# Performance work log

Hardware: AMD Instinct MI355X
Metric: run time of the kernel (lower is better)

The kernel has to match this reference:

```python
import jax, jax.numpy as jnp
import numpy as np

VOCAB, HIDDEN, BATCH, EMB, SEQ = 512, 512, 64, 256, 1024


def _lstm_cell(x, h, c, Wih, Whh, bih, bhh):
    # PyTorch LSTMCell gate order: i, f, g, o
    gates = x @ Wih.T + bih + h @ Whh.T + bhh  # [B, 4H]
    i, f, g, o = jnp.split(gates, 4, axis=-1)
    i = jax.nn.sigmoid(i)
    f = jax.nn.sigmoid(f)
    g = jnp.tanh(g)
    o = jax.nn.sigmoid(o)
    c_new = f * c + i * g
    h_new = o * jnp.tanh(c_new)
    return h_new, c_new


def setup_inputs() -> dict:
    key = jax.random.key(0)
    ks = jax.random.split(key, 12)
    s_e = 1.0 / np.sqrt(HIDDEN)
    inp = {
        "x": jax.random.randint(ks[0], (SEQ, BATCH), 0, VOCAB, dtype=jnp.int64)
        if jax.config.jax_enable_x64 else jax.random.randint(ks[0], (SEQ, BATCH), 0, VOCAB, dtype=jnp.int32),
        "h0": jnp.zeros((BATCH, HIDDEN), jnp.float32),
        "c0": jnp.zeros((BATCH, HIDDEN), jnp.float32),
        "emb": jax.random.normal(ks[1], (VOCAB, EMB), jnp.float32),
        "Wih1": jax.random.uniform(ks[2], (4 * HIDDEN, EMB), jnp.float32, -s_e, s_e),
        "Whh1": jax.random.uniform(ks[3], (4 * HIDDEN, HIDDEN), jnp.float32, -s_e, s_e),
        "bih1": jax.random.uniform(ks[4], (4 * HIDDEN,), jnp.float32, -s_e, s_e),
        "bhh1": jax.random.uniform(ks[5], (4 * HIDDEN,), jnp.float32, -s_e, s_e),
        "Wih2": jax.random.uniform(ks[6], (4 * HIDDEN, HIDDEN), jnp.float32, -s_e, s_e),
        "Whh2": jax.random.uniform(ks[7], (4 * HIDDEN, HIDDEN), jnp.float32, -s_e, s_e),
        "bih2": jax.random.uniform(ks[8], (4 * HIDDEN,), jnp.float32, -s_e, s_e),
        "bhh2": jax.random.uniform(ks[9], (4 * HIDDEN,), jnp.float32, -s_e, s_e),
        "Wfc": jax.random.uniform(ks[10], (VOCAB, HIDDEN), jnp.float32, -s_e, s_e),
        "bfc": jax.random.uniform(ks[11], (VOCAB,), jnp.float32, -s_e, s_e),
    }
    return inp


def reference(x, h0, c0, emb, Wih1, Whh1, bih1, bhh1, Wih2, Whh2, bih2, bhh2, Wfc, bfc):
    # Embedding lookup for the whole sequence: [S, B, E]
    x_emb = emb[x]

    def step(carry, xt):
        h1, c1, h2, c2 = carry
        h1, c1 = _lstm_cell(xt, h1, c1, Wih1, Whh1, bih1, bhh1)
        h2, c2 = _lstm_cell(h1, h2, c2, Wih2, Whh2, bih2, bhh2)
        return (h1, c1, h2, c2), h2

    # Both layers start from the same (h0, c0), matching the original hc1, hc2 = (hc, hc)
    _, h2_seq = jax.lax.scan(step, (h0, c0, h0, c0), x_emb)  # [S, B, H]
    # Dropout is identity in eval mode; output projection over all timesteps at once.
    out = jnp.einsum('sbh,vh->sbv', h2_seq, Wfc) + bfc  # [S, B, V]
    return out
```

## Files before the change

kernel.cpp:

```cpp
#include <hip/hip_runtime.h>

#define SEQn   1024
#define BATCHn 64
#define EMBn   256
#define HIDn   512
#define VOCn   512

#define NGRP 4
#define NL1g 16
#define NL2g 16
#define NFCg 16
#define GBLK (NL1g + NL2g + NFCg)
#define NBLK (NGRP * GBLK)
#define NPHASE (SEQn + 2)
#define HS 8192

using f16   = _Float16;
using half8 = __attribute__((ext_vector_type(8))) _Float16;
using f32x4 = __attribute__((ext_vector_type(4))) float;
using i32x4 = __attribute__((ext_vector_type(4))) int;

#define WS_FLG 0
#define WS_H1  4096
#define WS_H2  (WS_H1 + NGRP * 4 * HS * 2)
#define WS_P1  (WS_H2 + NGRP * 4 * HS * 2)


__device__ __forceinline__ float sigm_(float v) { return 1.0f / (1.0f + __expf(-v)); }
__device__ __forceinline__ float tanh_(float v) { return 1.0f - 2.0f / (__expf(2.0f * v) + 1.0f); }

__device__ __forceinline__ void st_b128_sc1(f16* p, f32x4 v) {
  asm volatile("global_store_dwordx4 %0, %1, off sc1" :: "v"(p), "v"(v) : "memory");
}

__device__ __forceinline__ void ld2_sc1(const f16* base, half8 (&a)[2]) {
  f32x4 t0, t1;
  asm volatile(
    "global_load_dwordx4 %0, %2, off sc1\n\t"
    "global_load_dwordx4 %1, %2, off offset:1024 sc1\n\t"
    "s_waitcnt vmcnt(0)"
    : "=&v"(t0), "=&v"(t1) : "v"(base) : "memory");
  a[0] = __builtin_bit_cast(half8, t0);
  a[1] = __builtin_bit_cast(half8, t1);
}
__device__ __forceinline__ void ld4_sc1(const f16* base, half8 (&a)[4]) {
  f32x4 t0, t1, t2, t3;
  asm volatile(
    "global_load_dwordx4 %0, %4, off sc1\n\t"
    "global_load_dwordx4 %1, %4, off offset:1024 sc1\n\t"
    "global_load_dwordx4 %2, %4, off offset:2048 sc1\n\t"
    "global_load_dwordx4 %3, %4, off offset:3072 sc1\n\t"
    "s_waitcnt vmcnt(0)"
    : "=&v"(t0), "=&v"(t1), "=&v"(t2), "=&v"(t3) : "v"(base) : "memory");
  a[0] = __builtin_bit_cast(half8, t0);
  a[1] = __builtin_bit_cast(half8, t1);
  a[2] = __builtin_bit_cast(half8, t2);
  a[3] = __builtin_bit_cast(half8, t3);
}

__global__ void k_init(const float* __restrict__ h0, char* __restrict__ ws) {
  int i = blockIdx.x * 256 + threadIdx.x;
  f16* h1b = (f16*)(ws + WS_H1);
  f16* h2b = (f16*)(ws + WS_H2);
  int slice = i >> 13;
  int off = i & (HS - 1);
  int g = slice >> 2;
  int ks = off >> 9, rem = off & 511;
  int qq = rem >> 7, cc = (rem >> 3) & 15, e = rem & 7;
  int row = g * 16 + cc, col = ks * 32 + qq * 8 + e;
  f16 v = (f16)h0[row * HIDn + col];
  h1b[i] = v;
  h2b[i] = v;
  if (i < 1024) ((int*)ws)[i] = 0;
}

__global__ void k_p1(const float* __restrict__ emb, const float* __restrict__ Wih1,
                     const float* __restrict__ bih1, const float* __restrict__ bhh1,
                     char* __restrict__ ws) {
  __shared__ float elds[32 * 256];
  int tid = threadIdx.x;
  int vb = blockIdx.x >> 5, gb = blockIdx.x & 31;
  for (int i = tid; i < 32 * 256; i += 256) elds[i] = emb[vb * 32 * 256 + i];
  __syncthreads();
  int gl = tid & 63, vs = tid >> 6;
  int g = gb * 64 + gl;
  float bias = bih1[g] + bhh1[g];
  float acc[8];
#pragma unroll
  for (int r = 0; r < 8; ++r) acc[r] = bias;
  const float* wrow = Wih1 + g * EMBn;
#pragma unroll 4
  for (int e = 0; e < EMBn; ++e) {
    float w = wrow[e];
#pragma unroll
    for (int r = 0; r < 8; ++r) acc[r] += elds[(vs * 8 + r) * 256 + e] * w;
  }
  f16* P1 = (f16*)(ws + WS_P1);
#pragma unroll
  for (int r = 0; r < 8; ++r) P1[(vb * 32 + vs * 8 + r) * 2048 + g] = (f16)acc[r];
}

__global__ void __launch_bounds__(512, 2)
k_lstm(const int* __restrict__ x, const float* __restrict__ c0,
       const float* __restrict__ Whh1,
       const float* __restrict__ Wih2, const float* __restrict__ Whh2,
       const float* __restrict__ bih2, const float* __restrict__ bhh2,
       const float* __restrict__ Wfc, const float* __restrict__ bfc,
       float* __restrict__ out, char* __restrict__ ws)
{
  __shared__ float part[8][16][132];
  __shared__ alignas(16) f16 hstage[16][32];

  const int bid = blockIdx.x, tid = threadIdx.x;
  const int lane = tid & 63, wv = tid >> 6;
  const int cc = lane & 15, qq = lane >> 4;
  const int group = bid / GBLK, role = bid % GBLK;
  const int rp = role & 1;

  f16* h1g = (f16*)(ws + WS_H1) + group * 4 * HS;
  f16* h2g = (f16*)(ws + WS_H2) + group * 4 * HS;
  const f16* P1 = (const f16*)(ws + WS_P1);
  int* flagp = (int*)ws + (group << 6) + role;

  half8 bfr[32];
  float cst = 0.f;
  float biasr[4] = {0.f, 0.f, 0.f, 0.f};
  float bfcr = 0.f;
  float pgf[4] = {0.f, 0.f, 0.f, 0.f};
  int j0 = 0;
  const int erow = tid >> 5, eu = tid & 31;

  if (role < NL1g) {
    j0 = role * 32;
#pragma unroll
    for (int nt = 0; nt < 8; ++nt) {
      const float* wr = Whh1 + ((nt >> 1) * 512 + j0 + (nt & 1) * 16 + cc) * HIDn;
#pragma unroll
      for (int kk = 0; kk < 2; ++kk) {
        const float* s = wr + (wv * 2 + kk) * 32 + qq * 8;
        half8 hv;
#pragma unroll
        for (int j = 0; j < 8; ++j) hv[j] = (f16)s[j];
        bfr[nt * 2 + kk] = hv;
      }
    }
    cst = c0[(group * 16 + erow) * HIDn + j0 + eu];
    {
      const f16* pr = P1 + (size_t)x[group * 16 + erow] * 2048 + j0 + eu;
#pragma unroll
      for (int g = 0; g < 4; ++g) pgf[g] = (float)pr[g * 512];
    }
  } else if (role < NL1g + NL2g) {
    j0 = (role - NL1g) * 32;
    const int kh = wv >> 2, kq = wv & 3;
    const float* W = kh ? Whh2 : Wih2;
#pragma unroll
    for (int nt = 0; nt < 8; ++nt) {
      const float* wr = W + ((nt >> 1) * 512 + j0 + (nt & 1) * 16 + cc) * HIDn;
#pragma unroll
      for (int kk = 0; kk < 4; ++kk) {
        const float* s = wr + (kq * 4 + kk) * 32 + qq * 8;
        half8 hv;
#pragma unroll
        for (int j = 0; j < 8; ++j) hv[j] = (f16)s[j];
        bfr[nt * 4 + kk] = hv;
      }
    }
#pragma unroll
    for (int g = 0; g < 4; ++g)
      biasr[g] = bih2[g * 512 + j0 + eu] + bhh2[g * 512 + j0 + eu];
    cst = c0[(group * 16 + erow) * HIDn + j0 + eu];
  } else {
    j0 = (role - NL1g - NL2g) * 32;
#pragma unroll
    for (int nt = 0; nt < 2; ++nt) {
      const float* wr = Wfc + (j0 + nt * 16 + cc) * HIDn;
#pragma unroll
      for (int kk = 0; kk < 2; ++kk) {
        const float* s = wr + (wv * 2 + kk) * 32 + qq * 8;
        half8 hv;
#pragma unroll
        for (int j = 0; j < 8; ++j) hv[j] = (f16)s[j];
        bfr[nt * 2 + kk] = hv;
      }
    }
    bfcr = bfc[j0 + eu];
  }
  const int ks0 = j0 >> 5;
  __syncthreads();

  for (int p = 1; p <= NPHASE; ++p) {
    if (role < NL1g) {
      if (p <= SEQn) {
        const f16* hp = h1g + (((p - 1) & 1) * 2 + rp) * HS;
        half8 a[2];
        ld2_sc1(hp + wv * 1024 + lane * 8, a);
        f32x4 acc[8];
#pragma unroll
        for (int nt = 0; nt < 8; ++nt)
#pragma unroll
          for (int r = 0; r < 4; ++r) acc[nt][r] = 0.f;
#pragma unroll
        for (int kk = 0; kk < 2; ++kk)
#pragma unroll
          for (int nt = 0; nt < 8; ++nt)
            acc[nt] = __builtin_amdgcn_mfma_f32_16x16x32_f16(a[kk], bfr[nt * 2 + kk], acc[nt], 0, 0, 0);
#pragma unroll
        for (int nt = 0; nt < 8; ++nt)
#pragma unroll
          for (int r = 0; r < 4; ++r)
            part[wv][qq * 4 + r][nt * 16 + cc] = acc[nt][r];
        __syncthreads();
        {
          float gs[4];
#pragma unroll
          for (int g = 0; g < 4; ++g) {
            float s = pgf[g];
#pragma unroll
            for (int kw = 0; kw < 8; ++kw) s += part[kw][erow][g * 32 + eu];
            gs[g] = s;
          }
          float cn = sigm_(gs[1]) * cst + sigm_(gs[0]) * tanh_(gs[2]);
          cst = cn;
          hstage[erow][eu] = (f16)(sigm_(gs[3]) * tanh_(cn));
        }
        __syncthreads();
        if (tid < 64) {
          f32x4 w = *(const f32x4*)&hstage[tid & 15][(tid >> 4) * 8];
          f16* ho = h1g + ((p & 1) * 2) * HS + ks0 * 512 + tid * 8;
          st_b128_sc1(ho, w);
          st_b128_sc1(ho + HS, w);
        }
      }
    } else if (role < NL1g + NL2g) {
      if (p >= 2 && p <= SEQn + 1) {
        const int kh = wv >> 2, kq = wv & 3;
        const f16* src = kh ? h2g + ((p & 1) * 2 + rp) * HS
                            : h1g + (((p - 1) & 1) * 2 + rp) * HS;
        half8 a[4];
        ld4_sc1(src + kq * 2048 + lane * 8, a);
        f32x4 acc[8];
#pragma unroll
        for (int nt = 0; nt < 8; ++nt)
#pragma unroll
          for (int r = 0; r < 4; ++r) acc[nt][r] = 0.f;
#pragma unroll
        for (int kk = 0; kk < 4; ++kk)
#pragma unroll
          for (int nt = 0; nt < 8; ++nt)
            acc[nt] = __builtin_amdgcn_mfma_f32_16x16x32_f16(a[kk], bfr[nt * 4 + kk], acc[nt], 0, 0, 0);
#pragma unroll
        for (int nt = 0; nt < 8; ++nt)
#pragma unroll
          for (int r = 0; r < 4; ++r)
            part[wv][qq * 4 + r][nt * 16 + cc] = acc[nt][r];
        __syncthreads();
        {
          float gs[4];
#pragma unroll
          for (int g = 0; g < 4; ++g) {
            float s = biasr[g];
#pragma unroll
            for (int kw = 0; kw < 8; ++kw) s += part[kw][erow][g * 32 + eu];
            gs[g] = s;
          }
          float cn = sigm_(gs[1]) * cst + sigm_(gs[0]) * tanh_(gs[2]);
          cst = cn;
          hstage[erow][eu] = (f16)(sigm_(gs[3]) * tanh_(cn));
        }
        __syncthreads();
        if (tid < 64) {
          f32x4 w = *(const f32x4*)&hstage[tid & 15][(tid >> 4) * 8];
          f16* ho = h2g + (((p - 1) & 1) * 2) * HS + ks0 * 512 + tid * 8;
          st_b128_sc1(ho, w);
          st_b128_sc1(ho + HS, w);
        }
      }
    } else {
      if (p >= 3) {
        const f16* hp = h2g + ((p & 1) * 2 + rp) * HS;
        half8 a[2];
        ld2_sc1(hp + wv * 1024 + lane * 8, a);
        f32x4 acc[2];
#pragma unroll
        for (int nt = 0; nt < 2; ++nt)
#pragma unroll
          for (int r = 0; r < 4; ++r) acc[nt][r] = 0.f;
#pragma unroll
        for (int kk = 0; kk < 2; ++kk)
#pragma unroll
          for (int nt = 0; nt < 2; ++nt)
            acc[nt] = __builtin_amdgcn_mfma_f32_16x16x32_f16(a[kk], bfr[nt * 2 + kk], acc[nt], 0, 0, 0);
#pragma unroll
        for (int nt = 0; nt < 2; ++nt)
#pragma unroll
          for (int r = 0; r < 4; ++r)
            part[wv][qq * 4 + r][nt * 16 + cc] = acc[nt][r];
        __syncthreads();
        {
          float s = bfcr;
#pragma unroll
          for (int kw = 0; kw < 8; ++kw) s += part[kw][erow][eu];
          float* op = out + (size_t)(p - 3) * (BATCHn * VOCn)
                    + (group * 16 + erow) * VOCn + j0 + eu;
          __builtin_nontemporal_store(s, op);
        }
      }
    }

    if (tid == 0) {
      asm volatile("s_waitcnt vmcnt(0)" ::: "memory");
      asm volatile("global_store_dword %0, %1, off sc1" :: "v"(flagp), "v"(p) : "memory");
    }
    if (role < NL1g && p < SEQn) {
      const f16* pr = P1 + (size_t)x[p * 64 + group * 16 + erow] * 2048 + j0 + eu;
#pragma unroll
      for (int g = 0; g < 4; ++g) pgf[g] = (float)pr[g * 512];
    }
    if (wv == 0) {
      const int* fp = (const int*)ws + (group << 6) + (lane << 2);
      for (;;) {
        i32x4 f;
        asm volatile("global_load_dwordx4 %0, %1, off sc1\n\ts_waitcnt vmcnt(0)"
                     : "=v"(f) : "v"(fp) : "memory");
        int ok = (lane >= 12) ||
                 ((f[0] >= p) & (f[1] >= p) & (f[2] >= p) & (f[3] >= p));
        if (__all(ok)) break;
        __builtin_amdgcn_s_sleep(4);
      }
    }
    __syncthreads();
  }
}

extern "C" void kernel_launch(void* const* d_in, const int* in_sizes, int n_in,
                              void* d_out, int out_size, void* d_ws, size_t ws_size,
                              hipStream_t stream) {
  (void)in_sizes; (void)n_in; (void)out_size; (void)ws_size;
  const int*   x    = (const int*)  d_in[0];
  const float* h0   = (const float*)d_in[1];
  const float* c0   = (const float*)d_in[2];
  const float* emb  = (const float*)d_in[3];
  const float* Wih1 = (const float*)d_in[4];
  const float* Whh1 = (const float*)d_in[5];
  const float* bih1 = (const float*)d_in[6];
  const float* bhh1 = (const float*)d_in[7];
  const float* Wih2 = (const float*)d_in[8];
  const float* Whh2 = (const float*)d_in[9];
  const float* bih2 = (const float*)d_in[10];
  const float* bhh2 = (const float*)d_in[11];
  const float* Wfc  = (const float*)d_in[12];
  const float* bfc  = (const float*)d_in[13];
  char* ws = (char*)d_ws;

  hipLaunchKernelGGL(k_init, dim3(512), dim3(256), 0, stream, h0, ws);
  hipLaunchKernelGGL(k_p1,   dim3(512), dim3(256), 0, stream, emb, Wih1, bih1, bhh1, ws);
  hipLaunchKernelGGL(k_lstm, dim3(NBLK), dim3(512), 0, stream,
                     x, c0, Whh1, Wih2, Whh2, bih2, bhh2, Wfc, bfc,
                     (float*)d_out, ws);
}
```

Measured before the change: 5.304 ms.

## Relax per-phase barrier to role-specific dependencies with 4-slot hidden-state ring

Replaces the all-blocks-wait-on-all barrier with per-role dependency thresholds, so each role waits only on the producers it needs and lets consumers lag by up to two phases. The hidden-state double buffers become a 4-slot ring so that producers can run ahead without overwriting data still being read. It also drops the store drain before the FC blocks' flag write and shortens the spin sleep. This aims to cut barrier stall per timestep. In exchange it costs more workspace and adds subtle correctness risk from the slack.

```diff
diff --git a/kernel.cpp b/kernel.cpp
--- a/kernel.cpp
+++ b/kernel.cpp
@@ -14,6 +14,8 @@
 #define NBLK (NGRP * GBLK)
 #define NPHASE (SEQn + 2)
 #define HS 8192
+#define NSLOT 4
+#define THR_IGN (-1)
 
 using f16   = _Float16;
 using half8 = __attribute__((ext_vector_type(8))) _Float16;
@@ -22,8 +24,8 @@
 
 #define WS_FLG 0
 #define WS_H1  4096
-#define WS_H2  (WS_H1 + NGRP * 4 * HS * 2)
-#define WS_P1  (WS_H2 + NGRP * 4 * HS * 2)
+#define WS_H2  (WS_H1 + NGRP * NSLOT * 2 * HS * 2)
+#define WS_P1  (WS_H2 + NGRP * NSLOT * 2 * HS * 2)
 
 
 __device__ __forceinline__ float sigm_(float v) { return 1.0f / (1.0f + __expf(-v)); }
@@ -62,16 +64,16 @@
   int i = blockIdx.x * 256 + threadIdx.x;
   f16* h1b = (f16*)(ws + WS_H1);
   f16* h2b = (f16*)(ws + WS_H2);
-  int slice = i >> 13;
+  int g = i >> 13;
   int off = i & (HS - 1);
-  int g = slice >> 2;
   int ks = off >> 9, rem = off & 511;
   int qq = rem >> 7, cc = (rem >> 3) & 15, e = rem & 7;
   int row = g * 16 + cc, col = ks * 32 + qq * 8 + e;
   f16 v = (f16)h0[row * HIDn + col];
-  h1b[i] = v;
-  h2b[i] = v;
-  if (i < 1024) ((int*)ws)[i] = 0;
+  int base = g * (NSLOT * 2 * HS);
+  h1b[base + off] = v;  h1b[base + HS + off] = v;
+  h2b[base + off] = v;  h2b[base + HS + off] = v;
+  if (i < 256) ((int*)ws)[i] = 0;
 }
 
 __global__ void k_p1(const float* __restrict__ emb, const float* __restrict__ Wih1,
@@ -115,12 +117,12 @@
   const int lane = tid & 63, wv = tid >> 6;
   const int cc = lane & 15, qq = lane >> 4;
   const int group = bid / GBLK, role = bid % GBLK;
-  const int rp = role & 1;
-
-  f16* h1g = (f16*)(ws + WS_H1) + group * 4 * HS;
-  f16* h2g = (f16*)(ws + WS_H2) + group * 4 * HS;
+
+  f16* h1g = (f16*)(ws + WS_H1) + group * (NSLOT * 2 * HS);
+  f16* h2g = (f16*)(ws + WS_H2) + group * (NSLOT * 2 * HS);
   const f16* P1 = (const f16*)(ws + WS_P1);
-  int* flagp = (int*)ws + (group << 6) + role;
+  const int cls = (role < NL1g) ? 0 : (role < NL1g + NL2g) ? 1 : 2;
+  int* flagp = (int*)ws + (group << 6) + (cls << 4) + (role & 15);
 
   half8 bfr[32];
   float cst = 0.f;
@@ -130,7 +132,7 @@
   int j0 = 0;
   const int erow = tid >> 5, eu = tid & 31;
 
-  if (role < NL1g) {
+  if (cls == 0) {
     j0 = role * 32;
 #pragma unroll
     for (int nt = 0; nt < 8; ++nt) {
@@ -150,7 +152,7 @@
 #pragma unroll
       for (int g = 0; g < 4; ++g) pgf[g] = (float)pr[g * 512];
     }
-  } else if (role < NL1g + NL2g) {
+  } else if (cls == 1) {
     j0 = (role - NL1g) * 32;
     const int kh = wv >> 2, kq = wv & 3;
     const float* W = kh ? Whh2 : Wih2;
@@ -190,9 +192,9 @@
   __syncthreads();
 
   for (int p = 1; p <= NPHASE; ++p) {
-    if (role < NL1g) {
+    if (cls == 0) {
       if (p <= SEQn) {
-        const f16* hp = h1g + (((p - 1) & 1) * 2 + rp) * HS;
+        const f16* hp = h1g + ((p - 1) & 3) * (2 * HS);
         half8 a[2];
         ld2_sc1(hp + wv * 1024 + lane * 8, a);
         f32x4 acc[8];
@@ -227,16 +229,16 @@
         __syncthreads();
         if (tid < 64) {
           f32x4 w = *(const f32x4*)&hstage[tid & 15][(tid >> 4) * 8];
-          f16* ho = h1g + ((p & 1) * 2) * HS + ks0 * 512 + tid * 8;
+          f16* ho = h1g + (p & 3) * (2 * HS) + ks0 * 512 + tid * 8;
           st_b128_sc1(ho, w);
           st_b128_sc1(ho + HS, w);
         }
       }
-    } else if (role < NL1g + NL2g) {
+    } else if (cls == 1) {
       if (p >= 2 && p <= SEQn + 1) {
         const int kh = wv >> 2, kq = wv & 3;
-        const f16* src = kh ? h2g + ((p & 1) * 2 + rp) * HS
-                            : h1g + (((p - 1) & 1) * 2 + rp) * HS;
+        const f16* src = kh ? h2g + ((p - 2) & 3) * (2 * HS)
+                            : h1g + ((p - 1) & 3) * (2 * HS) + HS;
         half8 a[4];
         ld4_sc1(src + kq * 2048 + lane * 8, a);
         f32x4 acc[8];
@@ -271,14 +273,14 @@
         __syncthreads();
         if (tid < 64) {
           f32x4 w = *(const f32x4*)&hstage[tid & 15][(tid >> 4) * 8];
-          f16* ho = h2g + (((p - 1) & 1) * 2) * HS + ks0 * 512 + tid * 8;
+          f16* ho = h2g + ((p - 1) & 3) * (2 * HS) + ks0 * 512 + tid * 8;
           st_b128_sc1(ho, w);
           st_b128_sc1(ho + HS, w);
         }
       }
     } else {
       if (p >= 3) {
-        const f16* hp = h2g + ((p & 1) * 2 + rp) * HS;
+        const f16* hp = h2g + ((p - 2) & 3) * (2 * HS) + HS;
         half8 a[2];
         ld2_sc1(hp + wv * 1024 + lane * 8, a);
         f32x4 acc[2];
@@ -309,24 +311,30 @@
     }
 
     if (tid == 0) {
-      asm volatile("s_waitcnt vmcnt(0)" ::: "memory");
+      if (cls != 2) asm volatile("s_waitcnt vmcnt(0)" ::: "memory");
       asm volatile("global_store_dword %0, %1, off sc1" :: "v"(flagp), "v"(p) : "memory");
     }
-    if (role < NL1g && p < SEQn) {
+    if (cls == 0 && p < SEQn) {
       const f16* pr = P1 + (size_t)x[p * 64 + group * 16 + erow] * 2048 + j0 + eu;
 #pragma unroll
       for (int g = 0; g < 4; ++g) pgf[g] = (float)pr[g * 512];
     }
     if (wv == 0) {
-      const int* fp = (const int*)ws + (group << 6) + (lane << 2);
+      int line = lane >> 2;
+      int lc = (line < 3) ? line : 0;
+      const int* fp = (const int*)ws + (group << 6) + (lc << 4) + ((lane & 3) << 2);
+      int thr;
+      if (cls == 0)      thr = (line == 0) ? p : (line == 1 ? p - 2 : THR_IGN);
+      else if (cls == 1) thr = (line == 0) ? p : (line == 1 ? p : (line == 2 ? p - 2 : THR_IGN));
+      else               thr = (line == 1) ? p : THR_IGN;
+      if (line >= 3) thr = THR_IGN;
       for (;;) {
         i32x4 f;
         asm volatile("global_load_dwordx4 %0, %1, off sc1\n\ts_waitcnt vmcnt(0)"
                      : "=v"(f) : "v"(fp) : "memory");
-        int ok = (lane >= 12) ||
-                 ((f[0] >= p) & (f[1] >= p) & (f[2] >= p) & (f[3] >= p));
+        int ok = (f[0] >= thr) & (f[1] >= thr) & (f[2] >= thr) & (f[3] >= thr);
         if (__all(ok)) break;
-        __builtin_amdgcn_s_sleep(4);
+        __builtin_amdgcn_s_sleep(1);
       }
     }
     __syncthreads();
@@ -353,7 +361,7 @@
   const float* bfc  = (const float*)d_in[13];
   char* ws = (char*)d_ws;
 
-  hipLaunchKernelGGL(k_init, dim3(512), dim3(256), 0, stream, h0, ws);
+  hipLaunchKernelGGL(k_init, dim3(128), dim3(256), 0, stream, h0, ws);
   hipLaunchKernelGGL(k_p1,   dim3(512), dim3(256), 0, stream, emb, Wih1, bih1, bhh1, ws);
   hipLaunchKernelGGL(k_lstm, dim3(NBLK), dim3(512), 0, stream,
                      x, c0, Whh1, Wih2, Whh2, bih2, bhh2, Wfc, bfc,
```

New measurement: 4.951 ms. 6.6% less time.
